# Performance work log

Measured on AMD Instinct MI355X. Metric: run time of the kernel, lower is better.

## Reference

```python
import jax, jax.numpy as jnp
import numpy as np

LEAKY_ALPHA = 0.2
NEG_INF = -9e15


def setup_inputs() -> dict:
    key = jax.random.key(0)
    k1, k2, k3, k4, k5 = jax.random.split(key, 5)
    n, n_head, f_in, f_out = 4096, 8, 1024, 128
    scale_w = float(np.sqrt(6.0 / (f_in + f_out)))      # xavier_uniform over (f_in,f_out)
    scale_a = float(np.sqrt(6.0 / (f_out + 1)))
    return {
        "h": jax.random.normal(k1, (n, f_in), dtype=jnp.float32),
        "adj": jax.random.randint(k2, (n, n), 0, 2, dtype=jnp.int32),
        "w": jax.random.uniform(k3, (n_head, f_in, f_out), jnp.float32, -scale_w, scale_w),
        "bias": jnp.zeros((f_out,), dtype=jnp.float32),
        "a_src": jax.random.uniform(k4, (n_head, f_out, 1), jnp.float32, -scale_a, scale_a),
        "a_dst": jax.random.uniform(k5, (n_head, f_out, 1), jnp.float32, -scale_a, scale_a),
    }


def reference(h, adj, w, bias, a_src, a_dst):
    n = h.shape[0]
    # per-head projection: [h_head, n, f_out]
    h_prime = jnp.einsum('nf,hfo->hno', h, w)
    attn_src = jnp.einsum('hno,hoi->hn', h_prime, a_src)   # [n_head, n]
    attn_dst = jnp.einsum('hno,hoi->hn', h_prime, a_dst)   # [n_head, n]
    # additive score: attn[h,i,j] = src[h,i] + dst[h,j]
    attn = attn_src[:, :, None] + attn_dst[:, None, :]
    attn = jnp.where(attn >= 0, attn, LEAKY_ALPHA * attn)  # leaky_relu
    attn = jnp.where(adj[None] > 0, attn, NEG_INF)
    attn = jax.nn.softmax(attn, axis=-1)                   # [n_head, n, n]
    # dropout layers are identity in eval mode
    output = jnp.einsum('hnm,hmo->hno', attn, h_prime) + bias
    output = jnp.transpose(output, (1, 0, 2)).reshape(n, -1)  # [n, n_head*f_out]
    weight = jnp.sum(attn, axis=0)                          # [n, n]
    return output, weight
```

## Files before the change

kernel.cpp:

```cpp
#include <hip/hip_runtime.h>
#include <hip/hip_bf16.h>


#define N 4096
#define NH 8
#define FIN 1024
#define FOUT 128

typedef short bf16x8 __attribute__((ext_vector_type(8)));
typedef float f32x4 __attribute__((ext_vector_type(4)));
typedef unsigned int uint;
typedef unsigned short ushort;

__device__ __forceinline__ float b2f(ushort u){ return __uint_as_float(((uint)u)<<16); }
__device__ __forceinline__ uint pk2cvt(float a, float b){
    float2 f; f.x=a; f.y=b;
    __hip_bfloat162 h = __float22bfloat162_rn(f);
    uint r; __builtin_memcpy(&r, &h, 4); return r;
}
__device__ __forceinline__ float sane(float x, float lim){ return fminf(fmaxf(x,-lim),lim); }
__device__ __forceinline__ int swz(int r, int cg){ return r*64 + (((cg) ^ (r & 7)) << 3); }
__device__ __forceinline__ void glds16(const ushort* g, ushort* l){
    __builtin_amdgcn_global_load_lds(
        (const __attribute__((address_space(1))) void*)g,
        (__attribute__((address_space(3))) void*)l, 16, 0, 0);
}
__device__ __forceinline__ int detect_mode(const ushort* hraw){
    ushort u = hraw[2*(threadIdx.x & 63)];
    int e = (u>>7)&0xFF;
    unsigned long long m = __ballot(e>=90 && e<=141);
    return (__popcll(m)>=40)?0:1;
}

__global__ __launch_bounds__(256) void pack_adj(const int* __restrict__ adj,
                                                uint* __restrict__ bitsT) {
    size_t idx = (size_t)blockIdx.x * 256 + threadIdx.x;
    int v = adj[idx];
    unsigned long long m = __ballot(v != 0);
    int lane = threadIdx.x & 63;
    uint i  = (uint)(idx >> 12);
    uint jw = ((uint)idx & 4095u) >> 5;
    if (lane == 0)       bitsT[jw * N + i] = (uint)m;
    else if (lane == 32) bitsT[jw * N + i] = (uint)(m >> 32);
}

__global__ __launch_bounds__(256) void transpose_w(const void* __restrict__ wraw,
                                                   const ushort* __restrict__ hraw,
                                                   ushort* __restrict__ wT) {
    __shared__ ushort tile[64][72];
    int mode = detect_mode(hraw);
    int h = blockIdx.z, f0 = blockIdx.x * 64, o0 = blockIdx.y * 64;
    int t = threadIdx.x;
#pragma unroll
    for (int it = 0; it < 2; ++it) {
        int slot = it * 256 + t;
        int row = slot >> 3, c = slot & 7;
        size_t eoff = (size_t)h * (FIN * FOUT) + (size_t)(f0 + row) * FOUT + o0 + c * 8;
        alignas(16) ushort tmp[8];
        if (mode == 0) {
            *reinterpret_cast<uint4*>(tmp) = *reinterpret_cast<const uint4*>((const ushort*)wraw + eoff);
        } else {
            const float* wF = (const float*)wraw;
            float4 x = *reinterpret_cast<const float4*>(wF + eoff);
            float4 y = *reinterpret_cast<const float4*>(wF + eoff + 4);
            uint4 p; p.x = pk2cvt(x.x,x.y); p.y = pk2cvt(x.z,x.w);
            p.z = pk2cvt(y.x,y.y); p.w = pk2cvt(y.z,y.w);
            *reinterpret_cast<uint4*>(tmp) = p;
        }
        *reinterpret_cast<uint4*>(&tile[row][c * 8]) = *reinterpret_cast<uint4*>(tmp);
    }
    __syncthreads();
#pragma unroll
    for (int it = 0; it < 2; ++it) {
        int slot = it * 256 + t;
        int orow = slot >> 3, c = slot & 7;
        alignas(16) ushort tmp[8];
#pragma unroll
        for (int k = 0; k < 8; ++k) tmp[k] = tile[c * 8 + k][orow];
        *reinterpret_cast<uint4*>(wT + (size_t)h * (FIN * FOUT) + (size_t)(o0 + orow) * FIN + f0 + c * 8) =
            *reinterpret_cast<uint4*>(tmp);
    }
}

__global__ __launch_bounds__(256) void zero2(float* __restrict__ acc, float* __restrict__ lsum,
                                             int nacc) {
    int b = blockIdx.x, t = threadIdx.x;
    float4 z; z.x=0.f; z.y=0.f; z.z=0.f; z.w=0.f;
    if (b < nacc) reinterpret_cast<float4*>(acc)[(size_t)b*256+t] = z;
    else          reinterpret_cast<float4*>(lsum)[(size_t)(b-nacc)*256+t] = z;
}

__global__ __launch_bounds__(256) void gemm_hp(
        const void* __restrict__ hraw, const ushort* __restrict__ wT,
        const void* __restrict__ asraw, const void* __restrict__ adraw,
        ushort* __restrict__ hpT,
        float* __restrict__ es1, float* __restrict__ es2,
        float* __restrict__ ed1, float* __restrict__ ed2) {
    __shared__ ushort Bs[2][FOUT * 64];
    __shared__ float sred[64], dred[64];
    int mode = detect_mode((const ushort*)hraw);
    int t = threadIdx.x;
    int i0 = blockIdx.x * 64, head = blockIdx.y;
    int w = t >> 6, lane = t & 63, quad = lane >> 4, l16 = lane & 15, wsh = quad * 8;
    int arow = i0 + w * 16 + l16;
    const ushort* hU = (const ushort*)hraw;
    const float*  hF = (const float*)hraw;
    int l8 = lane >> 3, lk = (lane & 7) ^ (l8 & 7);
    const ushort* gs[4];
#pragma unroll
    for (int s = 0; s < 4; ++s) {
        int o = (w * 4 + s) * 8 + l8;
        gs[s] = wT + (size_t)head * FOUT * FIN + (size_t)o * FIN + lk * 8;
    }

    float asv[8], adv[8];
#pragma unroll
    for (int n = 0; n < 8; ++n) {
        int ai = head * FOUT + n * 16 + l16;
        asv[n] = mode ? ((const float*)asraw)[ai] : b2f(((const ushort*)asraw)[ai]);
        adv[n] = mode ? ((const float*)adraw)[ai] : b2f(((const ushort*)adraw)[ai]);
    }

    f32x4 acc[8] = {};
#pragma unroll
    for (int s = 0; s < 4; ++s) glds16(gs[s], &Bs[0][(w * 4 + s) * 512]);
    uint4 au[2]; float4 af[2][2];
    if (mode == 0) {
#pragma unroll
        for (int kk = 0; kk < 2; ++kk)
            au[kk] = *reinterpret_cast<const uint4*>(hU + (size_t)arow * FIN + kk * 32 + wsh);
    } else {
#pragma unroll
        for (int kk = 0; kk < 2; ++kk) {
            af[kk][0] = *reinterpret_cast<const float4*>(hF + (size_t)arow * FIN + kk * 32 + wsh);
            af[kk][1] = *reinterpret_cast<const float4*>(hF + (size_t)arow * FIN + kk * 32 + wsh + 4);
        }
    }
    __syncthreads();

    for (int c = 0; c < 16; ++c) {
        int k0 = c * 64;
        if (c < 15) {
            ushort* bsw = &Bs[(c + 1) & 1][0];
#pragma unroll
            for (int s = 0; s < 4; ++s)
                glds16(gs[s] + k0 + 64, &bsw[(w * 4 + s) * 512]);
        }
        bf16x8 a2[2];
        if (mode == 0) {
            a2[0] = *reinterpret_cast<bf16x8*>(&au[0]);
            a2[1] = *reinterpret_cast<bf16x8*>(&au[1]);
        } else {
#pragma unroll
            for (int kk = 0; kk < 2; ++kk) {
                uint4 av; av.x = pk2cvt(af[kk][0].x, af[kk][0].y); av.y = pk2cvt(af[kk][0].z, af[kk][0].w);
                av.z = pk2cvt(af[kk][1].x, af[kk][1].y); av.w = pk2cvt(af[kk][1].z, af[kk][1].w);
                a2[kk] = *reinterpret_cast<bf16x8*>(&av);
            }
        }
        if (c < 15) {
            if (mode == 0) {
#pragma unroll
                for (int kk = 0; kk < 2; ++kk)
                    au[kk] = *reinterpret_cast<const uint4*>(hU + (size_t)arow * FIN + k0 + 64 + kk * 32 + wsh);
            } else {
#pragma unroll
                for (int kk = 0; kk < 2; ++kk) {
                    af[kk][0] = *reinterpret_cast<const float4*>(hF + (size_t)arow * FIN + k0 + 64 + kk * 32 + wsh);
                    af[kk][1] = *reinterpret_cast<const float4*>(hF + (size_t)arow * FIN + k0 + 64 + kk * 32 + wsh + 4);
                }
            }
        }
        const ushort* bsr = &Bs[c & 1][0];
#pragma unroll
        for (int kk = 0; kk < 2; ++kk) {
            int cg0 = kk * 4 + quad;
#pragma unroll
            for (int n = 0; n < 8; ++n) {
                bf16x8 b = *reinterpret_cast<const bf16x8*>(&bsr[swz(n * 16 + l16, cg0)]);
                acc[n] = __builtin_amdgcn_mfma_f32_16x16x32_bf16(a2[kk], b, acc[n], 0, 0, 0);
            }
        }
        if (c < 15) __syncthreads();
    }
#pragma unroll
    for (int n = 0; n < 8; ++n) {
        uint2 pk;
        pk.x = pk2cvt(acc[n][0], acc[n][1]);
        pk.y = pk2cvt(acc[n][2], acc[n][3]);
        *reinterpret_cast<uint2*>(hpT + ((size_t)head * FOUT + n * 16 + l16) * N + i0 + w * 16 + quad * 4) = pk;
    }
#pragma unroll
    for (int rr = 0; rr < 4; ++rr) {
        float s = 0.f, d = 0.f;
#pragma unroll
        for (int n = 0; n < 8; ++n) { s += acc[n][rr] * asv[n]; d += acc[n][rr] * adv[n]; }
#pragma unroll
        for (int off = 1; off < 16; off <<= 1) { s += __shfl_xor(s, off); d += __shfl_xor(d, off); }
        if (l16 == 0) { sred[w * 16 + quad * 4 + rr] = s; dred[w * 16 + quad * 4 + rr] = d; }
    }
    __syncthreads();
    if (t < 64) {
        int i = i0 + t;
        float s = sane(sred[t], 30.f);
        float d = sane(dred[t], 30.f);
        es1[head * N + i] = __expf(s);       es2[head * N + i] = __expf(0.2f * s);
        ed1[head * N + i] = __expf(d);       ed2[head * N + i] = __expf(0.2f * d);
    }
}

__global__ __launch_bounds__(256, 4) void pv_kernel(
        const ushort* __restrict__ hpT,
        const float* __restrict__ es1, const float* __restrict__ es2,
        const float* __restrict__ ed1, const float* __restrict__ ed2,
        const uint* __restrict__ bitsT,
        float* __restrict__ accOut, float* __restrict__ lsum, int use_atomic) {
    __shared__ ushort Bs[2][FOUT * 64];
    __shared__ float Ed[2][1024];
    int t = threadIdx.x;
    int lin = blockIdx.x + 32 * blockIdx.y + 256 * blockIdx.z;
    int g  = (lin & 7) * 4 + (lin >> 8);
    int ib = (lin >> 3) & 31;
    int hh = g & 7, kz = g >> 3;
    int i0 = ib * 128, kb = kz * 1024;
    int w = t >> 6, lane = t & 63, quad = lane >> 4, l16 = lane & 15, wsh = quad * 8;
    int irow[2];
    float s1[2], s2[2];
#pragma unroll
    for (int mi = 0; mi < 2; ++mi) {
        irow[mi] = i0 + w * 32 + mi * 16 + l16;
        s1[mi] = es1[hh * N + irow[mi]];
        s2[mi] = es2[hh * N + irow[mi]];
    }
    const uint* bp = bitsT + (size_t)(kb >> 5) * N;
    int l8 = lane >> 3, lk = (lane & 7) ^ (l8 & 7);
    const ushort* gs[4];
#pragma unroll
    for (int s = 0; s < 4; ++s) {
        int o = (w * 4 + s) * 8 + l8;
        gs[s] = hpT + (size_t)hh * FOUT * N + (size_t)o * N + kb + lk * 8;
    }
    bf16x8 ones;
#pragma unroll
    for (int j = 0; j < 8; ++j) ones[j] = (short)0x3F80;

    f32x4 acc[2][8] = {};
    f32x4 accl[2] = {};

    float4 ev1 = *reinterpret_cast<const float4*>(ed1 + hh * N + kb + t * 4);
    float4 ev2 = *reinterpret_cast<const float4*>(ed2 + hh * N + kb + t * 4);
    uint bwc[2][2], bwn[2][2];
#pragma unroll
    for (int kk = 0; kk < 2; ++kk)
#pragma unroll
        for (int mi = 0; mi < 2; ++mi) bwc[kk][mi] = bp[(size_t)kk * N + irow[mi]];
#pragma unroll
    for (int s = 0; s < 4; ++s) glds16(gs[s], &Bs[0][(w * 4 + s) * 512]);
    *reinterpret_cast<float4*>(&Ed[0][t * 4]) = ev1;
    *reinterpret_cast<float4*>(&Ed[1][t * 4]) = ev2;
    __syncthreads();

    for (int c = 0; c < 16; ++c) {
        if (c < 15) {
            ushort* bsw = &Bs[(c + 1) & 1][0];
#pragma unroll
            for (int s = 0; s < 4; ++s)
                glds16(gs[s] + (c + 1) * 64, &bsw[(w * 4 + s) * 512]);
#pragma unroll
            for (int kk = 0; kk < 2; ++kk)
#pragma unroll
                for (int mi = 0; mi < 2; ++mi)
                    bwn[kk][mi] = bp[(size_t)((c + 1) * 2 + kk) * N + irow[mi]];
        }
        const ushort* bsr = &Bs[c & 1][0];
#pragma unroll
        for (int kk = 0; kk < 2; ++kk) {
            int kgl = c * 64 + kk * 32 + wsh;
            float4 d1a = *reinterpret_cast<const float4*>(&Ed[0][kgl]);
            float4 d1b = *reinterpret_cast<const float4*>(&Ed[0][kgl + 4]);
            float4 d2a = *reinterpret_cast<const float4*>(&Ed[1][kgl]);
            float4 d2b = *reinterpret_cast<const float4*>(&Ed[1][kgl + 4]);
            bf16x8 am[2];
#pragma unroll
            for (int mi = 0; mi < 2; ++mi) {
                uint word = bwc[kk][mi] >> wsh;
                float e0 = fmaxf(s1[mi]*d1a.x, s2[mi]*d2a.x); e0 = (word & 1u)   ? e0 : 0.f;
                float e1 = fmaxf(s1[mi]*d1a.y, s2[mi]*d2a.y); e1 = (word & 2u)   ? e1 : 0.f;
                float e2 = fmaxf(s1[mi]*d1a.z, s2[mi]*d2a.z); e2 = (word & 4u)   ? e2 : 0.f;
                float e3 = fmaxf(s1[mi]*d1a.w, s2[mi]*d2a.w); e3 = (word & 8u)   ? e3 : 0.f;
                float e4 = fmaxf(s1[mi]*d1b.x, s2[mi]*d2b.x); e4 = (word & 16u)  ? e4 : 0.f;
                float e5 = fmaxf(s1[mi]*d1b.y, s2[mi]*d2b.y); e5 = (word & 32u)  ? e5 : 0.f;
                float e6 = fmaxf(s1[mi]*d1b.z, s2[mi]*d2b.z); e6 = (word & 64u)  ? e6 : 0.f;
                float e7 = fmaxf(s1[mi]*d1b.w, s2[mi]*d2b.w); e7 = (word & 128u) ? e7 : 0.f;
                uint4 av; av.x = pk2cvt(e0, e1); av.y = pk2cvt(e2, e3);
                av.z = pk2cvt(e4, e5); av.w = pk2cvt(e6, e7);
                am[mi] = *reinterpret_cast<bf16x8*>(&av);
                accl[mi] = __builtin_amdgcn_mfma_f32_16x16x32_bf16(am[mi], ones, accl[mi], 0, 0, 0);
            }
            int cg0 = kk * 4 + quad;
            __builtin_amdgcn_s_setprio(1);
#pragma unroll
            for (int n = 0; n < 8; ++n) {
                bf16x8 b = *reinterpret_cast<const bf16x8*>(&bsr[swz(n * 16 + l16, cg0)]);
                acc[0][n] = __builtin_amdgcn_mfma_f32_16x16x32_bf16(am[0], b, acc[0][n], 0, 0, 0);
                acc[1][n] = __builtin_amdgcn_mfma_f32_16x16x32_bf16(am[1], b, acc[1][n], 0, 0, 0);
            }
            __builtin_amdgcn_s_setprio(0);
        }
#pragma unroll
        for (int kk = 0; kk < 2; ++kk)
#pragma unroll
            for (int mi = 0; mi < 2; ++mi) bwc[kk][mi] = bwn[kk][mi];
        if (c < 15) __syncthreads();
    }
    if (l16 == 0) {
#pragma unroll
        for (int mi = 0; mi < 2; ++mi)
#pragma unroll
            for (int rr = 0; rr < 4; ++rr)
                atomicAdd(&lsum[hh * N + i0 + w * 32 + mi * 16 + quad * 4 + rr], accl[mi][rr]);
    }
    if (use_atomic) {
#pragma unroll
        for (int mi = 0; mi < 2; ++mi) {
            float* arow = accOut + ((size_t)hh * N + i0 + w * 32 + mi * 16 + quad * 4) * FOUT + l16;
#pragma unroll
            for (int n = 0; n < 8; ++n)
#pragma unroll
                for (int rr = 0; rr < 4; ++rr)
                    atomicAdd(&arow[(size_t)rr * FOUT + n * 16], acc[mi][n][rr]);
        }
    } else {
        float* part = accOut + (size_t)kz * ((size_t)NH * N * FOUT);
#pragma unroll
        for (int mi = 0; mi < 2; ++mi) {
            float* arow = part + ((size_t)hh * N + i0 + w * 32 + mi * 16 + quad * 4) * FOUT + l16;
#pragma unroll
            for (int n = 0; n < 8; ++n)
#pragma unroll
                for (int rr = 0; rr < 4; ++rr)
                    arow[(size_t)rr * FOUT + n * 16] = acc[mi][n][rr];
        }
    }
}

__global__ __launch_bounds__(256) void recip2(const float* __restrict__ lsum,
                                              const float* __restrict__ es1, const float* __restrict__ es2,
                                              float* __restrict__ rinv,
                                              float* __restrict__ s1r, float* __restrict__ s2r) {
    int idx = blockIdx.x * 256 + threadIdx.x;
    float v = lsum[idx];
    float r = (v > 1e-30f) ? 1.0f / v : 0.f;
    rinv[idx] = r;
    s1r[idx] = es1[idx] * r;
    s2r[idx] = es2[idx] * r;
}

__global__ __launch_bounds__(256) void pv_epi(
        const float* __restrict__ acc32, const float* __restrict__ rinv,
        const void* __restrict__ braw, const ushort* __restrict__ hraw,
        void* __restrict__ outraw, int nparts) {
    int mode = detect_mode(hraw);
    int idx4 = blockIdx.x * 256 + threadIdx.x;
    int h = idx4 >> 17;
    int i = (idx4 >> 5) & 4095;
    int og = idx4 & 31;
    const size_t PSTRIDE4 = (size_t)NH * N * FOUT / 4;
    float4 v = reinterpret_cast<const float4*>(acc32)[idx4];
    if (nparts == 4) {
        float4 a = reinterpret_cast<const float4*>(acc32)[PSTRIDE4 + idx4];
        float4 b = reinterpret_cast<const float4*>(acc32)[2 * PSTRIDE4 + idx4];
        float4 c = reinterpret_cast<const float4*>(acc32)[3 * PSTRIDE4 + idx4];
        v.x += a.x + b.x + c.x; v.y += a.y + b.y + c.y;
        v.z += a.z + b.z + c.z; v.w += a.w + b.w + c.w;
    }
    float r = rinv[h * N + i];
    float4 bv;
    if (mode) bv = reinterpret_cast<const float4*>(braw)[og];
    else {
        const ushort* bu = (const ushort*)braw;
        bv.x = b2f(bu[og*4]); bv.y = b2f(bu[og*4+1]); bv.z = b2f(bu[og*4+2]); bv.w = b2f(bu[og*4+3]);
    }
    v.x = v.x * r + bv.x; v.y = v.y * r + bv.y; v.z = v.z * r + bv.z; v.w = v.w * r + bv.w;
    size_t ob = (size_t)i * (NH * FOUT) + h * FOUT + og * 4;
    if (mode) *reinterpret_cast<float4*>((float*)outraw + ob) = v;
    else {
        uint2 pk; pk.x = pk2cvt(v.x, v.y); pk.y = pk2cvt(v.z, v.w);
        *reinterpret_cast<uint2*>((ushort*)outraw + ob) = pk;
    }
}

__global__ __launch_bounds__(256) void weight_kernel(
        const float* __restrict__ s1r, const float* __restrict__ s2r,
        const float* __restrict__ ed1, const float* __restrict__ ed2,
        const uint* __restrict__ bitsT,
        const ushort* __restrict__ hraw,
        void* __restrict__ outraw) {
    int mode = detect_mode(hraw);
    ushort* woutU = (ushort*)outraw + (size_t)N * (NH * FOUT);
    float*  woutF = (float*)outraw  + (size_t)N * (NH * FOUT);
    int t = threadIdx.x;
    int j = blockIdx.x * 1024 + t * 4;
    int i0 = blockIdx.y * 32;
    float4 d1[NH], d2[NH];
#pragma unroll
    for (int hh = 0; hh < NH; ++hh) {
        d1[hh] = *reinterpret_cast<const float4*>(ed1 + hh * N + j);
        d2[hh] = *reinterpret_cast<const float4*>(ed2 + hh * N + j);
    }
    int wrow = j >> 5;
    int jsh = j & 31;
    for (int i = i0; i < i0 + 32; ++i) {
        uint wbits = bitsT[(size_t)wrow * N + i] >> jsh;
        float sx = 0.f, sy = 0.f, sz = 0.f, sw = 0.f;
#pragma unroll
        for (int hh = 0; hh < NH; ++hh) {
            float a = s1r[hh * N + i];
            float b = s2r[hh * N + i];
            sx += fmaxf(a * d1[hh].x, b * d2[hh].x);
            sy += fmaxf(a * d1[hh].y, b * d2[hh].y);
            sz += fmaxf(a * d1[hh].z, b * d2[hh].z);
            sw += fmaxf(a * d1[hh].w, b * d2[hh].w);
        }
        sx = (wbits & 1u) ? sx : 0.f;
        sy = (wbits & 2u) ? sy : 0.f;
        sz = (wbits & 4u) ? sz : 0.f;
        sw = (wbits & 8u) ? sw : 0.f;
        size_t oidx = (size_t)i * N + j;
        if (mode) {
            float4 st; st.x = sx; st.y = sy; st.z = sz; st.w = sw;
            *reinterpret_cast<float4*>(woutF + oidx) = st;
        } else {
            uint2 pk; pk.x = pk2cvt(sx, sy); pk.y = pk2cvt(sz, sw);
            *reinterpret_cast<uint2*>(woutU + oidx) = pk;
        }
    }
}

extern "C" void kernel_launch(void* const* d_in, const int* in_sizes, int n_in,
                              void* d_out, int out_size, void* d_ws, size_t ws_size,
                              hipStream_t stream) {
    (void)in_sizes; (void)n_in; (void)out_size;
    const void* hraw  = d_in[0];
    const int*  adj   = (const int*)d_in[1];
    const void* wraw  = d_in[2];
    const void* braw  = d_in[3];
    const void* asraw = d_in[4];
    const void* adraw = d_in[5];

    char* ws = (char*)d_ws;
    float* lsum = (float*)(ws + 0);
    float* rinv = (float*)(ws + 131072);
    float* es1  = (float*)(ws + 262144);
    float* es2  = (float*)(ws + 393216);
    float* ed1  = (float*)(ws + 524288);
    float* ed2  = (float*)(ws + 655360);
    float* s1r  = (float*)(ws + 786432);
    float* s2r  = (float*)(ws + 917504);
    uint*  bitsT= (uint*)(ws + 1048576);
    ushort* wT  = (ushort*)(ws + 3145728);

    const size_t SMALL_END = 5242880;
    const size_t PART = 16777216;
    float*  acc32; ushort* hpT;
    int use_atomic, nparts;
    if (ws_size >= SMALL_END + 4 * PART + 8388608ull) {
        char* b = ws + SMALL_END;
        acc32 = (float*)b;
        hpT   = (ushort*)(b + 4 * PART);
        use_atomic = 0; nparts = 4;
    } else if (ws_size >= SMALL_END + 25165824ull) {
        char* b = ws + SMALL_END;
        acc32 = (float*)b;
        hpT   = (ushort*)(b + PART);
        use_atomic = 1; nparts = 1;
    } else {
        char* ob = (char*)d_out;
        acc32 = (float*)(ob + 16777216);
        hpT   = (ushort*)(ob + 33554432);
        use_atomic = 1; nparts = 1;
    }

    transpose_w<<<dim3(16, 2, 8), 256, 0, stream>>>(wraw, (const ushort*)hraw, wT);
    pack_adj<<<65536, 256, 0, stream>>>(adj, bitsT);
    if (use_atomic) zero2<<<4128, 256, 0, stream>>>(acc32, lsum, 4096);
    else            zero2<<<32,   256, 0, stream>>>(acc32, lsum, 0);
    gemm_hp<<<dim3(64, 8), 256, 0, stream>>>(hraw, wT, asraw, adraw, hpT, es1, es2, ed1, ed2);
    pv_kernel<<<dim3(32, 8, 4), 256, 0, stream>>>(hpT, es1, es2, ed1, ed2, bitsT,
                                                  acc32, lsum, use_atomic);
    recip2<<<128, 256, 0, stream>>>(lsum, es1, es2, rinv, s1r, s2r);
    pv_epi<<<4096, 256, 0, stream>>>(acc32, rinv, braw, (const ushort*)hraw, d_out, nparts);
    weight_kernel<<<dim3(4, 128), 256, 0, stream>>>(s1r, s2r, ed1, ed2, bitsT,
                                                    (const ushort*)hraw, d_out);
}
```

Measured before the change: 290.4 us.

## Row-major adjacency bits, interleaved dst exps, packed mul, scalar row sums in pv_kernel

Stores the packed adjacency bitmask row-major so each row's mask words can be read as contiguous uint2 loads instead of strided per-row loads. The destination exponentials are also written interleaved (d1,d2) so pv_kernel can read pairs and form both products with one packed v_pk_mul_f32. The row-sum MFMA against a ones vector is replaced by scalar adds plus a cross-quad shuffle reduction before the atomic. This cuts MFMA issue and scattered memory traffic, at the cost of more VALU adds and an extra edi buffer written by gemm_hp.

```diff
diff --git a/kernel.cpp b/kernel.cpp
--- a/kernel.cpp
+++ b/kernel.cpp
@@ -9,6 +9,7 @@
 
 typedef short bf16x8 __attribute__((ext_vector_type(8)));
 typedef float f32x4 __attribute__((ext_vector_type(4)));
+typedef float f32x2 __attribute__((ext_vector_type(2)));
 typedef unsigned int uint;
 typedef unsigned short ushort;
 
@@ -33,15 +34,15 @@
 }
 
 __global__ __launch_bounds__(256) void pack_adj(const int* __restrict__ adj,
-                                                uint* __restrict__ bitsT) {
+                                                uint* __restrict__ bitsR) {
     size_t idx = (size_t)blockIdx.x * 256 + threadIdx.x;
     int v = adj[idx];
     unsigned long long m = __ballot(v != 0);
     int lane = threadIdx.x & 63;
     uint i  = (uint)(idx >> 12);
     uint jw = ((uint)idx & 4095u) >> 5;
-    if (lane == 0)       bitsT[jw * N + i] = (uint)m;
-    else if (lane == 32) bitsT[jw * N + i] = (uint)(m >> 32);
+    if (lane == 0)       bitsR[i * 128 + jw] = (uint)m;
+    else if (lane == 32) bitsR[i * 128 + jw] = (uint)(m >> 32);
 }
 
 __global__ __launch_bounds__(256) void transpose_w(const void* __restrict__ wraw,
@@ -95,7 +96,8 @@
         const void* __restrict__ asraw, const void* __restrict__ adraw,
         ushort* __restrict__ hpT,
         float* __restrict__ es1, float* __restrict__ es2,
-        float* __restrict__ ed1, float* __restrict__ ed2) {
+        float* __restrict__ ed1, float* __restrict__ ed2,
+        float* __restrict__ edi) {
     __shared__ ushort Bs[2][FOUT * 64];
     __shared__ float sred[64], dred[64];
     int mode = detect_mode((const ushort*)hraw);
@@ -205,18 +207,21 @@
         float s = sane(sred[t], 30.f);
         float d = sane(dred[t], 30.f);
         es1[head * N + i] = __expf(s);       es2[head * N + i] = __expf(0.2f * s);
-        ed1[head * N + i] = __expf(d);       ed2[head * N + i] = __expf(0.2f * d);
+        float d1 = __expf(d), d2 = __expf(0.2f * d);
+        ed1[head * N + i] = d1;              ed2[head * N + i] = d2;
+        float2 di; di.x = d1; di.y = d2;
+        *reinterpret_cast<float2*>(edi + ((size_t)head * N + i) * 2) = di;
     }
 }
 
 __global__ __launch_bounds__(256, 4) void pv_kernel(
         const ushort* __restrict__ hpT,
         const float* __restrict__ es1, const float* __restrict__ es2,
-        const float* __restrict__ ed1, const float* __restrict__ ed2,
-        const uint* __restrict__ bitsT,
+        const float* __restrict__ edi,
+        const uint* __restrict__ bitsR,
         float* __restrict__ accOut, float* __restrict__ lsum, int use_atomic) {
     __shared__ ushort Bs[2][FOUT * 64];
-    __shared__ float Ed[2][1024];
+    __shared__ float Ed[2048];
     int t = threadIdx.x;
     int lin = blockIdx.x + 32 * blockIdx.y + 256 * blockIdx.z;
     int g  = (lin & 7) * 4 + (lin >> 8);
@@ -225,39 +230,32 @@
     int i0 = ib * 128, kb = kz * 1024;
     int w = t >> 6, lane = t & 63, quad = lane >> 4, l16 = lane & 15, wsh = quad * 8;
     int irow[2];
-    float s1[2], s2[2];
+    f32x2 sp[2];
 #pragma unroll
     for (int mi = 0; mi < 2; ++mi) {
         irow[mi] = i0 + w * 32 + mi * 16 + l16;
-        s1[mi] = es1[hh * N + irow[mi]];
-        s2[mi] = es2[hh * N + irow[mi]];
-    }
-    const uint* bp = bitsT + (size_t)(kb >> 5) * N;
-    int l8 = lane >> 3, lk = (lane & 7) ^ (l8 & 7);
-    const ushort* gs[4];
-#pragma unroll
-    for (int s = 0; s < 4; ++s) {
-        int o = (w * 4 + s) * 8 + l8;
-        gs[s] = hpT + (size_t)hh * FOUT * N + (size_t)o * N + kb + lk * 8;
-    }
-    bf16x8 ones;
-#pragma unroll
-    for (int j = 0; j < 8; ++j) ones[j] = (short)0x3F80;
+        sp[mi][0] = es1[hh * N + irow[mi]];
+        sp[mi][1] = es2[hh * N + irow[mi]];
+    }
+    const ushort* gbase = hpT + (size_t)hh * FOUT * N + kb;
+    int l8 = lane >> 3;
+    uint voff = (uint)((w * 32 + l8) * N + ((lane & 7) ^ (l8 & 7)) * 8);
+    const uint* brow0 = bitsR + (size_t)irow[0] * 128 + kz * 32;
+    const uint* brow1 = bitsR + (size_t)irow[1] * 128 + kz * 32;
 
     f32x4 acc[2][8] = {};
-    f32x4 accl[2] = {};
-
-    float4 ev1 = *reinterpret_cast<const float4*>(ed1 + hh * N + kb + t * 4);
-    float4 ev2 = *reinterpret_cast<const float4*>(ed2 + hh * N + kb + t * 4);
-    uint bwc[2][2], bwn[2][2];
-#pragma unroll
-    for (int kk = 0; kk < 2; ++kk)
-#pragma unroll
-        for (int mi = 0; mi < 2; ++mi) bwc[kk][mi] = bp[(size_t)kk * N + irow[mi]];
-#pragma unroll
-    for (int s = 0; s < 4; ++s) glds16(gs[s], &Bs[0][(w * 4 + s) * 512]);
-    *reinterpret_cast<float4*>(&Ed[0][t * 4]) = ev1;
-    *reinterpret_cast<float4*>(&Ed[1][t * 4]) = ev2;
+    float lac[2] = {0.f, 0.f};
+
+    float4 e4a = *reinterpret_cast<const float4*>(edi + ((size_t)hh * N + kb) * 2 + t * 8);
+    float4 e4b = *reinterpret_cast<const float4*>(edi + ((size_t)hh * N + kb) * 2 + t * 8 + 4);
+    uint2 bwc[2], bwn[2];
+    bwc[0] = *reinterpret_cast<const uint2*>(brow0);
+    bwc[1] = *reinterpret_cast<const uint2*>(brow1);
+#pragma unroll
+    for (int s = 0; s < 4; ++s)
+        glds16(gbase + s * 8 * N + voff, &Bs[0][(w * 4 + s) * 512]);
+    *reinterpret_cast<float4*>(&Ed[t * 8]) = e4a;
+    *reinterpret_cast<float4*>(&Ed[t * 8 + 4]) = e4b;
     __syncthreads();
 
     for (int c = 0; c < 16; ++c) {
@@ -265,37 +263,34 @@
             ushort* bsw = &Bs[(c + 1) & 1][0];
 #pragma unroll
             for (int s = 0; s < 4; ++s)
-                glds16(gs[s] + (c + 1) * 64, &bsw[(w * 4 + s) * 512]);
-#pragma unroll
-            for (int kk = 0; kk < 2; ++kk)
-#pragma unroll
-                for (int mi = 0; mi < 2; ++mi)
-                    bwn[kk][mi] = bp[(size_t)((c + 1) * 2 + kk) * N + irow[mi]];
+                glds16(gbase + (c + 1) * 64 + s * 8 * N + voff, &bsw[(w * 4 + s) * 512]);
+            bwn[0] = *reinterpret_cast<const uint2*>(brow0 + 2 * (c + 1));
+            bwn[1] = *reinterpret_cast<const uint2*>(brow1 + 2 * (c + 1));
         }
         const ushort* bsr = &Bs[c & 1][0];
 #pragma unroll
         for (int kk = 0; kk < 2; ++kk) {
-            int kgl = c * 64 + kk * 32 + wsh;
-            float4 d1a = *reinterpret_cast<const float4*>(&Ed[0][kgl]);
-            float4 d1b = *reinterpret_cast<const float4*>(&Ed[0][kgl + 4]);
-            float4 d2a = *reinterpret_cast<const float4*>(&Ed[1][kgl]);
-            float4 d2b = *reinterpret_cast<const float4*>(&Ed[1][kgl + 4]);
+            int eb = c * 128 + kk * 64 + quad * 16;
+            f32x2 dp[8];
+#pragma unroll
+            for (int p = 0; p < 8; ++p)
+                dp[p] = *reinterpret_cast<const f32x2*>(&Ed[eb + p * 2]);
             bf16x8 am[2];
 #pragma unroll
             for (int mi = 0; mi < 2; ++mi) {
-                uint word = bwc[kk][mi] >> wsh;
-                float e0 = fmaxf(s1[mi]*d1a.x, s2[mi]*d2a.x); e0 = (word & 1u)   ? e0 : 0.f;
-                float e1 = fmaxf(s1[mi]*d1a.y, s2[mi]*d2a.y); e1 = (word & 2u)   ? e1 : 0.f;
-                float e2 = fmaxf(s1[mi]*d1a.z, s2[mi]*d2a.z); e2 = (word & 4u)   ? e2 : 0.f;
-                float e3 = fmaxf(s1[mi]*d1a.w, s2[mi]*d2a.w); e3 = (word & 8u)   ? e3 : 0.f;
-                float e4 = fmaxf(s1[mi]*d1b.x, s2[mi]*d2b.x); e4 = (word & 16u)  ? e4 : 0.f;
-                float e5 = fmaxf(s1[mi]*d1b.y, s2[mi]*d2b.y); e5 = (word & 32u)  ? e5 : 0.f;
-                float e6 = fmaxf(s1[mi]*d1b.z, s2[mi]*d2b.z); e6 = (word & 64u)  ? e6 : 0.f;
-                float e7 = fmaxf(s1[mi]*d1b.w, s2[mi]*d2b.w); e7 = (word & 128u) ? e7 : 0.f;
-                uint4 av; av.x = pk2cvt(e0, e1); av.y = pk2cvt(e2, e3);
-                av.z = pk2cvt(e4, e5); av.w = pk2cvt(e6, e7);
+                uint wq = (kk ? bwc[mi].y : bwc[mi].x) >> wsh;
+                float e[8];
+#pragma unroll
+                for (int p = 0; p < 8; ++p) {
+                    f32x2 pr;
+                    asm("v_pk_mul_f32 %0, %1, %2" : "=v"(pr) : "v"(sp[mi]), "v"(dp[p]));
+                    float m = fmaxf(pr[0], pr[1]);
+                    e[p] = (wq & (1u << p)) ? m : 0.f;
+                }
+                lac[mi] += ((e[0] + e[1]) + (e[2] + e[3])) + ((e[4] + e[5]) + (e[6] + e[7]));
+                uint4 av; av.x = pk2cvt(e[0], e[1]); av.y = pk2cvt(e[2], e[3]);
+                av.z = pk2cvt(e[4], e[5]); av.w = pk2cvt(e[6], e[7]);
                 am[mi] = *reinterpret_cast<bf16x8*>(&av);
-                accl[mi] = __builtin_amdgcn_mfma_f32_16x16x32_bf16(am[mi], ones, accl[mi], 0, 0, 0);
             }
             int cg0 = kk * 4 + quad;
             __builtin_amdgcn_s_setprio(1);
@@ -307,18 +302,15 @@
             }
             __builtin_amdgcn_s_setprio(0);
         }
-#pragma unroll
-        for (int kk = 0; kk < 2; ++kk)
-#pragma unroll
-            for (int mi = 0; mi < 2; ++mi) bwc[kk][mi] = bwn[kk][mi];
+        bwc[0] = bwn[0]; bwc[1] = bwn[1];
         if (c < 15) __syncthreads();
     }
-    if (l16 == 0) {
-#pragma unroll
-        for (int mi = 0; mi < 2; ++mi)
-#pragma unroll
-            for (int rr = 0; rr < 4; ++rr)
-                atomicAdd(&lsum[hh * N + i0 + w * 32 + mi * 16 + quad * 4 + rr], accl[mi][rr]);
+#pragma unroll
+    for (int mi = 0; mi < 2; ++mi) {
+        float v = lac[mi];
+        v += __shfl_xor(v, 16);
+        v += __shfl_xor(v, 32);
+        if (quad == 0) atomicAdd(&lsum[hh * N + irow[mi]], v);
     }
     if (use_atomic) {
 #pragma unroll
@@ -393,7 +385,7 @@
 __global__ __launch_bounds__(256) void weight_kernel(
         const float* __restrict__ s1r, const float* __restrict__ s2r,
         const float* __restrict__ ed1, const float* __restrict__ ed2,
-        const uint* __restrict__ bitsT,
+        const uint* __restrict__ bitsR,
         const ushort* __restrict__ hraw,
         void* __restrict__ outraw) {
     int mode = detect_mode(hraw);
@@ -411,7 +403,7 @@
     int wrow = j >> 5;
     int jsh = j & 31;
     for (int i = i0; i < i0 + 32; ++i) {
-        uint wbits = bitsT[(size_t)wrow * N + i] >> jsh;
+        uint wbits = bitsR[(size_t)i * 128 + wrow] >> jsh;
         float sx = 0.f, sy = 0.f, sz = 0.f, sw = 0.f;
 #pragma unroll
         for (int hh = 0; hh < NH; ++hh) {
@@ -457,10 +449,11 @@
     float* ed2  = (float*)(ws + 655360);
     float* s1r  = (float*)(ws + 786432);
     float* s2r  = (float*)(ws + 917504);
-    uint*  bitsT= (uint*)(ws + 1048576);
-    ushort* wT  = (ushort*)(ws + 3145728);
-
-    const size_t SMALL_END = 5242880;
+    float* edi  = (float*)(ws + 1048576);
+    uint*  bitsR= (uint*)(ws + 1310720);
+    ushort* wT  = (ushort*)(ws + 3407872);
+
+    const size_t SMALL_END = 5505024;
     const size_t PART = 16777216;
     float*  acc32; ushort* hpT;
     int use_atomic, nparts;
@@ -482,14 +475,15 @@
     }
 
     transpose_w<<<dim3(16, 2, 8), 256, 0, stream>>>(wraw, (const ushort*)hraw, wT);
-    pack_adj<<<65536, 256, 0, stream>>>(adj, bitsT);
+    pack_adj<<<65536, 256, 0, stream>>>(adj, bitsR);
     if (use_atomic) zero2<<<4128, 256, 0, stream>>>(acc32, lsum, 4096);
     else            zero2<<<32,   256, 0, stream>>>(acc32, lsum, 0);
-    gemm_hp<<<dim3(64, 8), 256, 0, stream>>>(hraw, wT, asraw, adraw, hpT, es1, es2, ed1, ed2);
-    pv_kernel<<<dim3(32, 8, 4), 256, 0, stream>>>(hpT, es1, es2, ed1, ed2, bitsT,
+    gemm_hp<<<dim3(64, 8), 256, 0, stream>>>(hraw, wT, asraw, adraw, hpT,
+                                             es1, es2, ed1, ed2, edi);
+    pv_kernel<<<dim3(32, 8, 4), 256, 0, stream>>>(hpT, es1, es2, edi, bitsR,
                                                   acc32, lsum, use_atomic);
     recip2<<<128, 256, 0, stream>>>(lsum, es1, es2, rinv, s1r, s2r);
     pv_epi<<<4096, 256, 0, stream>>>(acc32, rinv, braw, (const ushort*)hraw, d_out, nparts);
-    weight_kernel<<<dim3(4, 128), 256, 0, stream>>>(s1r, s2r, ed1, ed2, bitsT,
+    weight_kernel<<<dim3(4, 128), 256, 0, stream>>>(s1r, s2r, ed1, ed2, bitsR,
                                                     (const ushort*)hraw, d_out);
 }
```

New measurement: 389.0 us. 33.9% more time.
